# Kernel tuning notes

Measured on AMD Instinct MI355X. Metric: run time of the kernel, lower is better.

## Reference

```python
import jax, jax.numpy as jnp
import numpy as np

EPS = 1e-8

def setup_inputs() -> dict:
    key = jax.random.key(0)
    ks = jax.random.split(key, 8)
    B, D, N, F = 8192, 1024, 2048, 8
    d2 = D // 2
    # integer-valued data (IDF acts on integers)
    x = jnp.round(jax.random.normal(ks[0], (B, D), jnp.float32) * 5.0)
    s1 = 1.0 / np.sqrt(d2)
    s2 = 1.0 / np.sqrt(N)
    return {
        "x": x,
        "W1": jax.random.normal(ks[1], (F, d2, N), jnp.float32) * s1,
        "b1": jax.random.normal(ks[2], (F, N), jnp.float32) * 0.01,
        "W2": jax.random.normal(ks[3], (F, N, N), jnp.float32) * s2,
        "b2": jax.random.normal(ks[4], (F, N), jnp.float32) * 0.01,
        "W3": jax.random.normal(ks[5], (F, N, d2), jnp.float32) * s2,
        "b3": jax.random.normal(ks[6], (F, d2), jnp.float32) * 0.01,
        "mean": jnp.zeros((1, D), jnp.float32),
        "log_scale": jnp.ones((1, D), jnp.float32),
    }

def _st_round(v):
    # straight-through round: forward round, identity gradient
    return v + jax.lax.stop_gradient(jnp.round(v) - v)

def _flow(x, W1, b1, W2, b2, W3, b3):
    d2 = x.shape[1] // 2
    def step(z, p):
        w1, bb1, w2, bb2, w3, bb3 = p
        xa, xb = z[:, :d2], z[:, d2:]
        h = jax.nn.leaky_relu(xa @ w1 + bb1)          # [B, N]
        h = jax.nn.leaky_relu(h @ w2 + bb2)           # [B, N]
        t = h @ w3 + bb3                               # [B, d2]
        yb = xb + _st_round(t)
        z = jnp.concatenate([xa, yb], axis=1)[:, ::-1]  # coupling + flip permute
        return z, None
    z, _ = jax.lax.scan(step, x, (W1, b1, W2, b2, W3, b3))
    return z

def reference(x, W1, b1, W2, b2, W3, b3, mean, log_scale):
    z = _flow(x, W1, b1, W2, b2, W3, b3)
    # discretized logistic log-prior: log(sig((z+.5-m)/s) - sig((z-.5-m)/s))
    scale = jnp.exp(log_scale)
    la = jax.nn.log_sigmoid((z + 0.5 - mean) / scale)
    lb = jax.nn.log_sigmoid((z - 0.5 - mean) / scale)
    log_p = la + jnp.log(1.0 - jnp.exp(lb - la) + EPS)  # log_min_exp
    return -log_p.sum(axis=1).mean()  # reduction='avg'
```

## Files before the change

kernel.cpp:

```cpp
#include <hip/hip_runtime.h>
#include <hip/hip_bf16.h>
#include <cmath>


typedef __bf16 bf16_t;
typedef bf16_t bf16x8 __attribute__((ext_vector_type(8)));
typedef float floatx4 __attribute__((ext_vector_type(4)));

#define BQ 8192
#define DD 1024
#define D2 512
#define NH 2048
#define NF 8

__device__ __forceinline__ void gload_lds16(const void* g, void* l) {
    __builtin_amdgcn_global_load_lds(
        (__attribute__((address_space(1))) void*)g,
        (__attribute__((address_space(3))) void*)l, 16, 0, 0);
}

__global__ __launch_bounds__(256)
void transpose_bf16(const float* __restrict__ W, bf16_t* __restrict__ Wt,
                    int K, int N) {
    __shared__ float tile[32][33];
    size_t fo = (size_t)blockIdx.z * K * N;
    int n0 = blockIdx.x * 32, k0 = blockIdx.y * 32;
    int tx = threadIdx.x & 31, ty = threadIdx.x >> 5;
    for (int i = 0; i < 4; i++)
        tile[ty + i*8][tx] = W[fo + (size_t)(k0 + ty + i*8) * N + n0 + tx];
    __syncthreads();
    for (int i = 0; i < 4; i++)
        Wt[fo + (size_t)(n0 + ty + i*8) * K + k0 + tx] = (bf16_t)tile[tx][ty + i*8];
}

__global__ __launch_bounds__(256)
void copy_x(const float4* __restrict__ x, float4* __restrict__ S) {
    int idx = blockIdx.x * blockDim.x + threadIdx.x;
    S[idx] = x[idx];
}

__global__ __launch_bounds__(256)
void prep_A(const float* __restrict__ S, bf16_t* __restrict__ Ab) {
    int idx = blockIdx.x * blockDim.x + threadIdx.x;
    int m = idx >> 9;
    int j = idx & 511;
    Ab[idx] = (bf16_t)S[(size_t)m * DD + j];
}

template<int MODE, int K>
__global__ __launch_bounds__(256, 2)
void gemm_kernel(const bf16_t* __restrict__ A, const bf16_t* __restrict__ Bt,
                 const float* __restrict__ bias,
                 bf16_t* __restrict__ Cout, float* __restrict__ S,
                 bf16_t* __restrict__ Abn,
                 int N, int rflag)
{
    __shared__ __align__(16) bf16_t As[2][128 * 64];
    __shared__ __align__(16) bf16_t Bs[2][128 * 64];

    const int tid  = threadIdx.x;
    const int lane = tid & 63;
    const int wave = tid >> 6;
    const int wm   = wave >> 1;
    const int wn   = wave & 1;
    const int m0   = blockIdx.y * 128;
    const int n0   = blockIdx.x * 128;

    const int srow = tid >> 3;
    const int sq   = ((tid & 7) ^ (srow & 7)) * 8;
    const bf16_t* agp = A  + (size_t)(m0 + srow) * K + sq;
    const bf16_t* bgp = Bt + (size_t)(n0 + srow) * K + sq;

    floatx4 acc[4][4];
#pragma unroll
    for (int i = 0; i < 4; i++)
#pragma unroll
        for (int j = 0; j < 4; j++)
            acc[i][j] = (floatx4){0.f, 0.f, 0.f, 0.f};

    const int fr = lane & 15;
    const int fq = lane >> 4;
    const int fx = lane & 7;

#pragma unroll
    for (int u = 0; u < 4; u++) {
        gload_lds16(agp + (size_t)(u*32) * K, &As[0][u*2048 + tid*8]);
        gload_lds16(bgp + (size_t)(u*32) * K, &Bs[0][u*2048 + tid*8]);
    }
    agp += 64; bgp += 64;

    constexpr int T = K / 64;
#pragma unroll 2
    for (int it = 1; it < T; ++it) {
        __syncthreads();
        const int nb = it & 1;
        const int cb = nb ^ 1;
#pragma unroll
        for (int u = 0; u < 4; u++) {
            gload_lds16(agp + (size_t)(u*32) * K, &As[nb][u*2048 + tid*8]);
            gload_lds16(bgp + (size_t)(u*32) * K, &Bs[nb][u*2048 + tid*8]);
        }
        agp += 64; bgp += 64;

#pragma unroll
        for (int s = 0; s < 2; s++) {
            const int kc = ((s*4 + fq) ^ fx) * 8;
            bf16x8 af[4], bff[4];
#pragma unroll
            for (int i = 0; i < 4; i++)
                af[i] = *(const bf16x8*)&As[cb][(wm*64 + i*16 + fr) * 64 + kc];
#pragma unroll
            for (int j = 0; j < 4; j++)
                bff[j] = *(const bf16x8*)&Bs[cb][(wn*64 + j*16 + fr) * 64 + kc];
#pragma unroll
            for (int i = 0; i < 4; i++)
#pragma unroll
                for (int j = 0; j < 4; j++)
                    acc[i][j] = __builtin_amdgcn_mfma_f32_16x16x32_bf16(
                                    af[i], bff[j], acc[i][j], 0, 0, 0);
        }
    }
    __syncthreads();
    {
        const int cb = (T - 1) & 1;
#pragma unroll
        for (int s = 0; s < 2; s++) {
            const int kc = ((s*4 + fq) ^ fx) * 8;
            bf16x8 af[4], bff[4];
#pragma unroll
            for (int i = 0; i < 4; i++)
                af[i] = *(const bf16x8*)&As[cb][(wm*64 + i*16 + fr) * 64 + kc];
#pragma unroll
            for (int j = 0; j < 4; j++)
                bff[j] = *(const bf16x8*)&Bs[cb][(wn*64 + j*16 + fr) * 64 + kc];
#pragma unroll
            for (int i = 0; i < 4; i++)
#pragma unroll
                for (int j = 0; j < 4; j++)
                    acc[i][j] = __builtin_amdgcn_mfma_f32_16x16x32_bf16(
                                    af[i], bff[j], acc[i][j], 0, 0, 0);
        }
    }

    const int ccol  = lane & 15;
    const int crow4 = (lane >> 4) * 4;
#pragma unroll
    for (int j = 0; j < 4; j++) {
        int col = n0 + wn*64 + j*16 + ccol;
        float bj = bias[col];
        if (MODE == 0) {
#pragma unroll
            for (int i = 0; i < 4; i++) {
#pragma unroll
                for (int r = 0; r < 4; r++) {
                    int row = m0 + wm*64 + i*16 + crow4 + r;
                    float v = acc[i][j][r] + bj;
                    v = v >= 0.f ? v : 0.01f * v;
                    Cout[(size_t)row * N + col] = (bf16_t)v;
                }
            }
        } else {
            int slot = rflag ? (511 - col) : (512 + col);
            int aj   = 511 - col;
#pragma unroll
            for (int i = 0; i < 4; i++) {
#pragma unroll
                for (int r = 0; r < 4; r++) {
                    int row = m0 + wm*64 + i*16 + crow4 + r;
                    float t = acc[i][j][r] + bj;
                    float nv = S[(size_t)row * DD + slot] + rintf(t);
                    S[(size_t)row * DD + slot] = nv;
                    Abn[(size_t)row * D2 + aj] = (bf16_t)nv;
                }
            }
        }
    }
}

__global__ __launch_bounds__(256)
void reduce_nll(const float* __restrict__ S, const float* __restrict__ mean,
                const float* __restrict__ log_scale, float* __restrict__ out)
{
    float local = 0.f;
    const int total = BQ * DD;
    for (int idx = blockIdx.x * blockDim.x + threadIdx.x; idx < total;
         idx += gridDim.x * blockDim.x) {
        int j = idx & (DD - 1);
        float z  = S[idx];
        float mu = mean[j];
        float sc = expf(log_scale[j]);
        float ua = (z + 0.5f - mu) / sc;
        float ub = (z - 0.5f - mu) / sc;
        float la = fminf(ua, 0.f) - log1pf(expf(-fabsf(ua)));
        float lb = fminf(ub, 0.f) - log1pf(expf(-fabsf(ub)));
        float lp = la + logf(1.0f - expf(lb - la) + 1e-8f);
        local += lp;
    }
    __shared__ float red[256];
    red[threadIdx.x] = local;
    __syncthreads();
    for (int s = 128; s > 0; s >>= 1) {
        if (threadIdx.x < s) red[threadIdx.x] += red[threadIdx.x + s];
        __syncthreads();
    }
    if (threadIdx.x == 0) atomicAdd(out, -red[0] * (1.0f / (float)BQ));
}

extern "C" void kernel_launch(void* const* d_in, const int* in_sizes, int n_in,
                              void* d_out, int out_size, void* d_ws, size_t ws_size,
                              hipStream_t stream)
{
    const float* x   = (const float*)d_in[0];
    const float* W1  = (const float*)d_in[1];
    const float* b1  = (const float*)d_in[2];
    const float* W2  = (const float*)d_in[3];
    const float* b2  = (const float*)d_in[4];
    const float* W3  = (const float*)d_in[5];
    const float* b3  = (const float*)d_in[6];
    const float* mean = (const float*)d_in[7];
    const float* lsc  = (const float*)d_in[8];

    char* ws = (char*)d_ws;
    bf16_t* Wt1 = (bf16_t*)ws; ws += (size_t)NF * NH * D2 * 2;
    bf16_t* Wt2 = (bf16_t*)ws; ws += (size_t)NF * NH * NH * 2;
    bf16_t* Wt3 = (bf16_t*)ws; ws += (size_t)NF * D2 * NH * 2;
    float*  S   = (float*)ws;  ws += (size_t)BQ * DD * 4;
    bf16_t* Ab  = (bf16_t*)ws; ws += (size_t)BQ * D2 * 2;
    bf16_t* H1  = (bf16_t*)ws; ws += (size_t)BQ * NH * 2;
    bf16_t* H2  = (bf16_t*)ws;

    hipMemsetAsync(d_out, 0, sizeof(float), stream);

    dim3 blk(256);
    transpose_bf16<<<dim3(NH/32, D2/32, NF), blk, 0, stream>>>(W1, Wt1, D2, NH);
    transpose_bf16<<<dim3(NH/32, NH/32, NF), blk, 0, stream>>>(W2, Wt2, NH, NH);
    transpose_bf16<<<dim3(D2/32, NH/32, NF), blk, 0, stream>>>(W3, Wt3, NH, D2);

    copy_x<<<BQ * DD / 4 / 256, blk, 0, stream>>>((const float4*)x, (float4*)S);
    prep_A<<<BQ * D2 / 256, blk, 0, stream>>>(S, Ab);

    for (int f = 0; f < NF; ++f) {
        int r = f & 1;
        gemm_kernel<0, D2><<<dim3(NH/128, BQ/128), blk, 0, stream>>>(
            Ab, Wt1 + (size_t)f * NH * D2, b1 + (size_t)f * NH, H1, nullptr,
            nullptr, NH, 0);
        gemm_kernel<0, NH><<<dim3(NH/128, BQ/128), blk, 0, stream>>>(
            H1, Wt2 + (size_t)f * NH * NH, b2 + (size_t)f * NH, H2, nullptr,
            nullptr, NH, 0);
        gemm_kernel<1, NH><<<dim3(D2/128, BQ/128), blk, 0, stream>>>(
            H2, Wt3 + (size_t)f * D2 * NH, b3 + (size_t)f * D2, nullptr, S,
            Ab, D2, r);
    }

    reduce_nll<<<2048, blk, 0, stream>>>(S, mean, lsc, (float*)d_out);
}
```

Measured before the change: 1.619 ms.

## Triple-buffer GEMM with BK=32, vmcnt waits, and smaller M tile for third GEMM

Replaces the double-buffered BK=64 GEMM main loop with a three-stage LDS ring at BK=32. It uses explicit s_waitcnt on outstanding global-to-LDS loads plus a single barrier per step, so tile loads overlap compute more deeply. It also templates the M tile size so the narrow third GEMM uses 64-row tiles for more blocks, and raises the occupancy hint to 3 blocks per CU. The risks are more barriers per unit of K, half-sized MFMA work per step, and correctness depending on the hand-written vmcnt encoding and the single-barrier buffer-reuse ordering.

```diff
diff --git a/kernel.cpp b/kernel.cpp
--- a/kernel.cpp
+++ b/kernel.cpp
@@ -47,100 +47,98 @@
     Ab[idx] = (bf16_t)S[(size_t)m * DD + j];
 }
 
-template<int MODE, int K>
-__global__ __launch_bounds__(256, 2)
+template<int MODE, int K, int TM>
+__global__ __launch_bounds__(256, 3)
 void gemm_kernel(const bf16_t* __restrict__ A, const bf16_t* __restrict__ Bt,
                  const float* __restrict__ bias,
                  bf16_t* __restrict__ Cout, float* __restrict__ S,
                  bf16_t* __restrict__ Abn,
                  int N, int rflag)
 {
-    __shared__ __align__(16) bf16_t As[2][128 * 64];
-    __shared__ __align__(16) bf16_t Bs[2][128 * 64];
+    constexpr int IM   = TM / 32;
+    constexpr int NA   = TM / 64;
+    constexpr int NDMA = NA + 2;
+    constexpr int T    = K / 32;
+    static_assert((T - 1) % 3 == 0, "pipeline triple-unroll needs (T-1)%3==0");
+
+    __shared__ __align__(16) bf16_t As[3][TM * 32];
+    __shared__ __align__(16) bf16_t Bs[3][128 * 32];
 
     const int tid  = threadIdx.x;
     const int lane = tid & 63;
     const int wave = tid >> 6;
     const int wm   = wave >> 1;
     const int wn   = wave & 1;
-    const int m0   = blockIdx.y * 128;
+    const int m0   = blockIdx.y * TM;
     const int n0   = blockIdx.x * 128;
 
-    const int srow = tid >> 3;
-    const int sq   = ((tid & 7) ^ (srow & 7)) * 8;
+    const int srow = tid >> 2;
+    const int sq   = ((tid & 3) ^ ((srow >> 1) & 3)) * 8;
     const bf16_t* agp = A  + (size_t)(m0 + srow) * K + sq;
     const bf16_t* bgp = Bt + (size_t)(n0 + srow) * K + sq;
 
-    floatx4 acc[4][4];
-#pragma unroll
-    for (int i = 0; i < 4; i++)
+    floatx4 acc[IM][4];
+#pragma unroll
+    for (int i = 0; i < IM; i++)
 #pragma unroll
         for (int j = 0; j < 4; j++)
             acc[i][j] = (floatx4){0.f, 0.f, 0.f, 0.f};
 
-    const int fr = lane & 15;
-    const int fq = lane >> 4;
-    const int fx = lane & 7;
-
-#pragma unroll
-    for (int u = 0; u < 4; u++) {
-        gload_lds16(agp + (size_t)(u*32) * K, &As[0][u*2048 + tid*8]);
-        gload_lds16(bgp + (size_t)(u*32) * K, &Bs[0][u*2048 + tid*8]);
-    }
-    agp += 64; bgp += 64;
-
-    constexpr int T = K / 64;
-#pragma unroll 2
-    for (int it = 1; it < T; ++it) {
-        __syncthreads();
-        const int nb = it & 1;
-        const int cb = nb ^ 1;
-#pragma unroll
-        for (int u = 0; u < 4; u++) {
-            gload_lds16(agp + (size_t)(u*32) * K, &As[nb][u*2048 + tid*8]);
-            gload_lds16(bgp + (size_t)(u*32) * K, &Bs[nb][u*2048 + tid*8]);
-        }
-        agp += 64; bgp += 64;
-
-#pragma unroll
-        for (int s = 0; s < 2; s++) {
-            const int kc = ((s*4 + fq) ^ fx) * 8;
-            bf16x8 af[4], bff[4];
-#pragma unroll
-            for (int i = 0; i < 4; i++)
-                af[i] = *(const bf16x8*)&As[cb][(wm*64 + i*16 + fr) * 64 + kc];
-#pragma unroll
-            for (int j = 0; j < 4; j++)
-                bff[j] = *(const bf16x8*)&Bs[cb][(wn*64 + j*16 + fr) * 64 + kc];
-#pragma unroll
-            for (int i = 0; i < 4; i++)
-#pragma unroll
-                for (int j = 0; j < 4; j++)
-                    acc[i][j] = __builtin_amdgcn_mfma_f32_16x16x32_bf16(
-                                    af[i], bff[j], acc[i][j], 0, 0, 0);
-        }
-    }
-    __syncthreads();
-    {
-        const int cb = (T - 1) & 1;
-#pragma unroll
-        for (int s = 0; s < 2; s++) {
-            const int kc = ((s*4 + fq) ^ fx) * 8;
-            bf16x8 af[4], bff[4];
-#pragma unroll
-            for (int i = 0; i < 4; i++)
-                af[i] = *(const bf16x8*)&As[cb][(wm*64 + i*16 + fr) * 64 + kc];
-#pragma unroll
-            for (int j = 0; j < 4; j++)
-                bff[j] = *(const bf16x8*)&Bs[cb][(wn*64 + j*16 + fr) * 64 + kc];
-#pragma unroll
-            for (int i = 0; i < 4; i++)
-#pragma unroll
-                for (int j = 0; j < 4; j++)
-                    acc[i][j] = __builtin_amdgcn_mfma_f32_16x16x32_bf16(
-                                    af[i], bff[j], acc[i][j], 0, 0, 0);
-        }
-    }
+    const int fr  = lane & 15;
+    const int fp8 = ((lane >> 4) ^ ((lane >> 1) & 3)) * 8;
+
+    bf16x8 af[IM], bff[4];
+
+#define ISSUE_TILE(NB)                                                       \
+    {                                                                        \
+        _Pragma("unroll")                                                    \
+        for (int u = 0; u < NA; u++)                                         \
+            gload_lds16(agp + (size_t)(u*64) * K, &As[NB][u*2048 + tid*8]);  \
+        _Pragma("unroll")                                                    \
+        for (int u = 0; u < 2; u++)                                          \
+            gload_lds16(bgp + (size_t)(u*64) * K, &Bs[NB][u*2048 + tid*8]);  \
+        agp += 32; bgp += 32;                                                \
+    }
+
+#define COMPUTE(CB)                                                          \
+    {                                                                        \
+        _Pragma("unroll")                                                    \
+        for (int i = 0; i < IM; i++)                                         \
+            af[i] = *(const bf16x8*)&As[CB][(wm*(TM/2) + i*16 + fr)*32 + fp8];\
+        _Pragma("unroll")                                                    \
+        for (int j = 0; j < 4; j++)                                          \
+            bff[j] = *(const bf16x8*)&Bs[CB][(wn*64 + j*16 + fr)*32 + fp8];  \
+        _Pragma("unroll")                                                    \
+        for (int i = 0; i < IM; i++)                                         \
+            _Pragma("unroll")                                                \
+            for (int j = 0; j < 4; j++)                                      \
+                acc[i][j] = __builtin_amdgcn_mfma_f32_16x16x32_bf16(         \
+                                af[i], bff[j], acc[i][j], 0, 0, 0);          \
+    }
+
+#define PIPE_STEP(NB, CB)                                                    \
+    {                                                                        \
+        ISSUE_TILE(NB);                                                      \
+        __builtin_amdgcn_s_waitcnt(0x0F70 | NDMA);     \
+        __builtin_amdgcn_s_barrier();                                        \
+        COMPUTE(CB);                                                         \
+    }
+
+    ISSUE_TILE(0);
+
+#pragma unroll 1
+    for (int g = 0; g < (T - 1) / 3; ++g) {
+        PIPE_STEP(1, 0);
+        PIPE_STEP(2, 1);
+        PIPE_STEP(0, 2);
+    }
+    __builtin_amdgcn_s_waitcnt(0x0F70);
+    __builtin_amdgcn_s_barrier();
+    COMPUTE(0);
+
+#undef PIPE_STEP
+#undef COMPUTE
+#undef ISSUE_TILE
 
     const int ccol  = lane & 15;
     const int crow4 = (lane >> 4) * 4;
@@ -150,10 +148,10 @@
         float bj = bias[col];
         if (MODE == 0) {
 #pragma unroll
-            for (int i = 0; i < 4; i++) {
+            for (int i = 0; i < IM; i++) {
 #pragma unroll
                 for (int r = 0; r < 4; r++) {
-                    int row = m0 + wm*64 + i*16 + crow4 + r;
+                    int row = m0 + wm*(TM/2) + i*16 + crow4 + r;
                     float v = acc[i][j][r] + bj;
                     v = v >= 0.f ? v : 0.01f * v;
                     Cout[(size_t)row * N + col] = (bf16_t)v;
@@ -163,10 +161,10 @@
             int slot = rflag ? (511 - col) : (512 + col);
             int aj   = 511 - col;
 #pragma unroll
-            for (int i = 0; i < 4; i++) {
+            for (int i = 0; i < IM; i++) {
 #pragma unroll
                 for (int r = 0; r < 4; r++) {
-                    int row = m0 + wm*64 + i*16 + crow4 + r;
+                    int row = m0 + wm*(TM/2) + i*16 + crow4 + r;
                     float t = acc[i][j][r] + bj;
                     float nv = S[(size_t)row * DD + slot] + rintf(t);
                     S[(size_t)row * DD + slot] = nv;
@@ -241,13 +239,13 @@
 
     for (int f = 0; f < NF; ++f) {
         int r = f & 1;
-        gemm_kernel<0, D2><<<dim3(NH/128, BQ/128), blk, 0, stream>>>(
+        gemm_kernel<0, D2, 128><<<dim3(NH/128, BQ/128), blk, 0, stream>>>(
             Ab, Wt1 + (size_t)f * NH * D2, b1 + (size_t)f * NH, H1, nullptr,
             nullptr, NH, 0);
-        gemm_kernel<0, NH><<<dim3(NH/128, BQ/128), blk, 0, stream>>>(
+        gemm_kernel<0, NH, 128><<<dim3(NH/128, BQ/128), blk, 0, stream>>>(
             H1, Wt2 + (size_t)f * NH * NH, b2 + (size_t)f * NH, H2, nullptr,
             nullptr, NH, 0);
-        gemm_kernel<1, NH><<<dim3(D2/128, BQ/128), blk, 0, stream>>>(
+        gemm_kernel<1, NH, 64><<<dim3(D2/128, BQ/64), blk, 0, stream>>>(
             H2, Wt3 + (size_t)f * D2 * NH, b3 + (size_t)f * D2, nullptr, S,
             Ab, D2, r);
     }
```

After: 1.617 ms. Within noise of the previous version (-0.1%).
